# Optimization experiments

Hardware: AMD Instinct MI355X
Metric: run time of the kernel (lower is better)

Reference implementation:

```python
import jax, jax.numpy as jnp
import numpy as np

N, E, H, L = 50000, 800000, 64, 4
IN_NODE, IN_EDGE = 16, 8


def _lin(x, W, b=None):
    y = x @ W
    return y if b is None else y + b


def setup_inputs() -> dict:
    key = jax.random.key(0)
    ks = jax.random.split(key, 32)
    r = lambda i, shp, s=0.1: jax.random.normal(ks[i], shp, dtype=jnp.float32) * s
    inp = {
        "h": r(0, (N, IN_NODE), 1.0),
        "x": r(1, (N, 3), 1.0),
        "edge_attr": r(2, (E, IN_EDGE), 1.0),
        "node_mask": jnp.ones((N, 1), jnp.float32),
        "edge_mask": jnp.ones((E, 1), jnp.float32),
        # embedding linears
        "Wn_in": r(3, (IN_NODE, H)), "bn_in": r(4, (H,)),
        "Wn_out": r(5, (H, IN_NODE)), "bn_out": r(6, (IN_NODE,)),
        "We_in": r(7, (IN_EDGE, H)), "be_in": r(8, (H,)),
        "We_out": r(9, (H, IN_EDGE)), "be_out": r(10, (IN_EDGE,)),
        # per-layer E_GCL params (stacked over L layers)
        "eW1": r(11, (L, 2 * H + 1 + H, H)), "eb1": r(12, (L, H)),
        "eW2": r(13, (L, H, H)), "eb2": r(14, (L, H)),
        "nW1": r(15, (L, 2 * H, H)), "nb1": r(16, (L, H)),
        "nW2": r(17, (L, H, H)), "nb2": r(18, (L, H)),
        "cW1": r(19, (L, H, H)), "cb1": r(20, (L, H)),
        "cW2": r(21, (L, H, 1)),
        "edge_index": jax.random.randint(ks[22], (2, E), 0, N, dtype=jnp.int32),
    }
    return inp


def reference(h, x, edge_attr, node_mask, edge_mask,
              Wn_in, bn_in, Wn_out, bn_out, We_in, be_in, We_out, be_out,
              eW1, eb1, eW2, eb2, nW1, nb1, nW2, nb2, cW1, cb1, cW2,
              edge_index):
    silu = jax.nn.silu
    n = h.shape[0]
    row, col = edge_index[0], edge_index[1]
    h = _lin(h, Wn_in, bn_in)            # node embedding [N,H]
    e = _lin(edge_attr, We_in, be_in)    # edge embedding [E,H]
    for i in range(eW1.shape[0]):        # n_layers (structural loop)
        coord_diff = x[row] - x[col]                          # [E,3]
        radial = jnp.sum(coord_diff * coord_diff, -1, keepdims=True)  # [E,1]
        coord_diff = coord_diff / (jnp.sqrt(radial) + 1.0)    # norm_diff
        # edge model: gather -> MLP
        m = jnp.concatenate([h[row], h[col], radial, e], axis=-1)
        m = silu(_lin(m, eW1[i], eb1[i]))
        m = silu(_lin(m, eW2[i], eb2[i]))
        m = m * edge_mask
        # coord model (tanh=False, agg='sum'): scatter-add translations
        trans = coord_diff * _lin(silu(_lin(m, cW1[i], cb1[i])), cW2[i])
        x = x + jax.ops.segment_sum(trans, row, num_segments=n)
        # node model: scatter-add messages, MLP, residual (recurrent)
        agg = jax.ops.segment_sum(m, row, num_segments=n)
        out = _lin(silu(_lin(jnp.concatenate([h, agg], -1), nW1[i], nb1[i])), nW2[i], nb2[i])
        h = (h + out) * node_mask
        x = x * node_mask
        e = m  # edge_update: carry message as updated edge feature
    e = _lin(e, We_out, be_out) * edge_mask
    h = _lin(h, Wn_out, bn_out) * node_mask
    return h, x, e
```

## Files before the change

### kernel.cpp

```cpp
#include <hip/hip_runtime.h>

#define N_NODES 50000
#define N_EDGES 800000
#define NLAYERS 4
#define NTILES (N_EDGES / 64)
#define NTILES2 (N_EDGES / 128)

#define K1PAD 224
#define TPITCH 72
#define SCHUNK 49

typedef short bf16x8 __attribute__((ext_vector_type(8)));
typedef float f32x4 __attribute__((ext_vector_type(4)));

__device__ __forceinline__ unsigned short f2b(float f) {
  union { float f; unsigned int u; } v; v.f = f;
  unsigned int u = v.u;
  return (unsigned short)((u + 0x7fffu + ((u >> 16) & 1u)) >> 16);
}
__device__ __forceinline__ float b2f(unsigned short s) {
  union { unsigned int u; float f; } v; v.u = ((unsigned int)s) << 16;
  return v.f;
}
__device__ __forceinline__ float silu_f(float x) {
  return x / (1.0f + __expf(-x));
}

__global__ void k_hist(const int* __restrict__ eidx, int* __restrict__ cnt) {
  int e = blockIdx.x * 256 + threadIdx.x;
  if (e >= N_EDGES) return;
  atomicAdd(&cnt[eidx[e]], 1);
}
__global__ __launch_bounds__(1024) void k_scan(const int* __restrict__ cnt,
                                               int* __restrict__ rowptr,
                                               int* __restrict__ cur) {
  __shared__ int part[1024];
  const int t = threadIdx.x;
  const int base = t * SCHUNK;
  int s = 0;
  for (int i = 0; i < SCHUNK; i++) {
    int idx = base + i;
    s += (idx < N_NODES) ? cnt[idx] : 0;
  }
  part[t] = s;
  __syncthreads();
  for (int off = 1; off < 1024; off <<= 1) {
    int v = (t >= off) ? part[t - off] : 0;
    __syncthreads();
    part[t] += v;
    __syncthreads();
  }
  int run = (t == 0) ? 0 : part[t - 1];
  for (int i = 0; i < SCHUNK; i++) {
    int idx = base + i;
    if (idx < N_NODES) {
      rowptr[idx] = run;
      cur[idx] = run;
      run += cnt[idx];
    }
  }
  if (t == 1023) rowptr[N_NODES] = part[1023];
}
__global__ void k_scatter(const int* __restrict__ eidx, const float* __restrict__ emask,
                          int* __restrict__ cur, int* __restrict__ elist,
                          int* __restrict__ rs, int* __restrict__ cs,
                          float* __restrict__ msrt) {
  int e = blockIdx.x * 256 + threadIdx.x;
  if (e >= N_EDGES) return;
  int r = eidx[e], c = eidx[N_EDGES + e];
  int slot = atomicAdd(&cur[r], 1);
  elist[slot] = e;
  rs[slot] = r;
  cs[slot] = c;
  msrt[slot] = emask[e];
}

__global__ void k_convW1(const float* __restrict__ eW1, unsigned short* __restrict__ Wt1) {
  int id = blockIdx.x * 256 + threadIdx.x;
  if (id >= NLAYERS * 64 * K1PAD) return;
  int k = id % K1PAD; int rem = id / K1PAD; int o = rem % 64; int l = rem / 64;
  int src = (k < 128) ? k : (k < 192 ? k + 1 : (k == 192 ? 128 : -1));
  float v = (src >= 0) ? eW1[((size_t)l * 193 + src) * 64 + o] : 0.0f;
  Wt1[id] = f2b(v);
}
__global__ void k_convT(const float* __restrict__ W, unsigned short* __restrict__ Wt, int K) {
  int id = blockIdx.x * 256 + threadIdx.x;
  if (id >= NLAYERS * 64 * K) return;
  int k = id % K; int rem = id / K; int o = rem % 64; int l = rem / 64;
  Wt[id] = f2b(W[((size_t)l * K + k) * 64 + o]);
}
__global__ void k_convHead(const float* __restrict__ W, unsigned short* __restrict__ Wt, int O) {
  int id = blockIdx.x * 256 + threadIdx.x;
  if (id >= 16 * 64) return;
  int k = id & 63, o = id >> 6;
  Wt[id] = (o < O) ? f2b(W[(size_t)k * O + o]) : (unsigned short)0;
}

__global__ void k_h0(const float* __restrict__ hin, const float* __restrict__ W,
                     const float* __restrict__ b, float* __restrict__ h,
                     unsigned short* __restrict__ hbf) {
  int id = blockIdx.x * 256 + threadIdx.x;
  if (id >= N_NODES * 64) return;
  int n = id >> 6, j = id & 63;
  float s = b[j];
#pragma unroll
  for (int k = 0; k < 16; k++) s += hin[n * 16 + k] * W[k * 64 + j];
  h[id] = s;
  hbf[id] = f2b(s);
}
__global__ void k_e0(const float* __restrict__ ea, const float* __restrict__ W,
                     const float* __restrict__ b, const int* __restrict__ elist,
                     unsigned short* __restrict__ ebuf) {
  int id = blockIdx.x * 256 + threadIdx.x;
  if (id >= N_EDGES * 64) return;
  int pos = id >> 6, j = id & 63;
  int e = elist[pos];
  float s = b[j];
#pragma unroll
  for (int k = 0; k < 8; k++) s += ea[e * 8 + k] * W[k * 64 + j];
  ebuf[id] = f2b(s);
}

__global__ __launch_bounds__(256) void edge_kernel(
    const unsigned short* __restrict__ hbf, unsigned short* __restrict__ ebuf,
    const float* __restrict__ xin, float* __restrict__ xout,
    float* __restrict__ agg,
    const int* __restrict__ rs, const int* __restrict__ cs,
    const float* __restrict__ msrt,
    const unsigned short* __restrict__ Wt1,
    const unsigned short* __restrict__ Wt2,
    const unsigned short* __restrict__ Wtc,
    const float* __restrict__ eb1, const float* __restrict__ eb2,
    const float* __restrict__ cb1, const float* __restrict__ cw2) {
  __shared__ __attribute__((aligned(16))) unsigned short sT[128 * TPITCH];
  __shared__ __attribute__((aligned(16))) unsigned short sM[128 * TPITCH];
  __shared__ float sNdx[128 * 3];
  __shared__ float sMaskS[128];
  __shared__ int sRow[128];

  const int t = threadIdx.x;
  const int lane = t & 63, w = t >> 6;
  const int q = lane >> 4, li = lane & 15;
  const int rowA = w * 32 + li;
  const int rowB = rowA + 16;
  const int e0 = blockIdx.x * 128 + rowA;
  const int e1 = e0 + 16;

  const int rA = rs[e0], cA = cs[e0];
  const int rB = rs[e1], cB = cs[e1];

  float radA = 0.f, radB = 0.f;
  if (q == 0) {
    {
      float dx0 = xin[rA * 3 + 0] - xin[cA * 3 + 0];
      float dx1 = xin[rA * 3 + 1] - xin[cA * 3 + 1];
      float dx2 = xin[rA * 3 + 2] - xin[cA * 3 + 2];
      radA = dx0 * dx0 + dx1 * dx1 + dx2 * dx2;
      float inv = 1.0f / (sqrtf(radA) + 1.0f);
      sRow[rowA] = rA;
      sMaskS[rowA] = msrt[e0];
      sNdx[rowA * 3 + 0] = dx0 * inv;
      sNdx[rowA * 3 + 1] = dx1 * inv;
      sNdx[rowA * 3 + 2] = dx2 * inv;
    }
    {
      float dx0 = xin[rB * 3 + 0] - xin[cB * 3 + 0];
      float dx1 = xin[rB * 3 + 1] - xin[cB * 3 + 1];
      float dx2 = xin[rB * 3 + 2] - xin[cB * 3 + 2];
      radB = dx0 * dx0 + dx1 * dx1 + dx2 * dx2;
      float inv = 1.0f / (sqrtf(radB) + 1.0f);
      sRow[rowB] = rB;
      sMaskS[rowB] = msrt[e1];
      sNdx[rowB * 3 + 0] = dx0 * inv;
      sNdx[rowB * 3 + 1] = dx1 * inv;
      sNdx[rowB * 3 + 2] = dx2 * inv;
    }
  }

  const unsigned short* hrA = hbf + (size_t)rA * 64;
  const unsigned short* hcA = hbf + (size_t)cA * 64;
  const unsigned short* epA = ebuf + (size_t)e0 * 64;
  const unsigned short* hrB = hbf + (size_t)rB * 64;
  const unsigned short* hcB = hbf + (size_t)cB * 64;
  const unsigned short* epB = ebuf + (size_t)e1 * 64;

  f32x4 accA[4], accB[4];
  const f32x4 zero4 = {0.f, 0.f, 0.f, 0.f};
#pragma unroll
  for (int ct = 0; ct < 4; ct++) { accA[ct] = zero4; accB[ct] = zero4; }

  {
    bf16x8 afA[7], afB[7];
    afA[0] = *(const bf16x8*)(hrA + q * 8);
    afA[1] = *(const bf16x8*)(hrA + 32 + q * 8);
    afA[2] = *(const bf16x8*)(hcA + q * 8);
    afA[3] = *(const bf16x8*)(hcA + 32 + q * 8);
    afA[4] = *(const bf16x8*)(epA + q * 8);
    afA[5] = *(const bf16x8*)(epA + 32 + q * 8);
    afB[0] = *(const bf16x8*)(hrB + q * 8);
    afB[1] = *(const bf16x8*)(hrB + 32 + q * 8);
    afB[2] = *(const bf16x8*)(hcB + q * 8);
    afB[3] = *(const bf16x8*)(hcB + 32 + q * 8);
    afB[4] = *(const bf16x8*)(epB + q * 8);
    afB[5] = *(const bf16x8*)(epB + 32 + q * 8);
    bf16x8 a6A = {0, 0, 0, 0, 0, 0, 0, 0};
    bf16x8 a6B = {0, 0, 0, 0, 0, 0, 0, 0};
    if (q == 0) { a6A[0] = (short)f2b(radA); a6B[0] = (short)f2b(radB); }
    afA[6] = a6A; afB[6] = a6B;
#pragma unroll
    for (int ks = 0; ks < 7; ks++) {
      int kb = ks * 32 + q * 8;
#pragma unroll
      for (int ct = 0; ct < 4; ct++) {
        bf16x8 bfr = *(const bf16x8*)(Wt1 + (size_t)(ct * 16 + li) * K1PAD + kb);
        accA[ct] = __builtin_amdgcn_mfma_f32_16x16x32_bf16(afA[ks], bfr, accA[ct], 0, 0, 0);
        accB[ct] = __builtin_amdgcn_mfma_f32_16x16x32_bf16(afB[ks], bfr, accB[ct], 0, 0, 0);
      }
    }
  }
#pragma unroll
  for (int ct = 0; ct < 4; ct++) {
    float bias = eb1[ct * 16 + li];
#pragma unroll
    for (int r2 = 0; r2 < 4; r2++) {
      int elA = w * 32 + q * 4 + r2;
      sT[elA * TPITCH + ct * 16 + li] = f2b(silu_f(accA[ct][r2] + bias));
      sT[(elA + 16) * TPITCH + ct * 16 + li] = f2b(silu_f(accB[ct][r2] + bias));
    }
  }

#pragma unroll
  for (int ct = 0; ct < 4; ct++) { accA[ct] = zero4; accB[ct] = zero4; }
#pragma unroll
  for (int ks = 0; ks < 2; ks++) {
    int kb = ks * 32 + q * 8;
    bf16x8 afA = *(const bf16x8*)(sT + rowA * TPITCH + kb);
    bf16x8 afB = *(const bf16x8*)(sT + rowB * TPITCH + kb);
#pragma unroll
    for (int ct = 0; ct < 4; ct++) {
      bf16x8 bfr = *(const bf16x8*)(Wt2 + (size_t)(ct * 16 + li) * 64 + kb);
      accA[ct] = __builtin_amdgcn_mfma_f32_16x16x32_bf16(afA, bfr, accA[ct], 0, 0, 0);
      accB[ct] = __builtin_amdgcn_mfma_f32_16x16x32_bf16(afB, bfr, accB[ct], 0, 0, 0);
    }
  }
#pragma unroll
  for (int ct = 0; ct < 4; ct++) {
    float bias = eb2[ct * 16 + li];
#pragma unroll
    for (int r2 = 0; r2 < 4; r2++) {
      int elA = w * 32 + q * 4 + r2;
      int elB = elA + 16;
      float vA = silu_f(accA[ct][r2] + bias) * sMaskS[elA];
      float vB = silu_f(accB[ct][r2] + bias) * sMaskS[elB];
      sM[elA * TPITCH + ct * 16 + li] = f2b(vA);
      sM[elB * TPITCH + ct * 16 + li] = f2b(vB);
    }
  }

  {
    int el2 = t >> 1, part = t & 1;
    const uint4* src = (const uint4*)(sM + el2 * TPITCH + part * 32);
    uint4* dst = (uint4*)(ebuf + (size_t)(blockIdx.x * 128 + el2) * 64 + part * 32);
    dst[0] = src[0]; dst[1] = src[1]; dst[2] = src[2]; dst[3] = src[3];
  }

  {
    float accv = 0.f;
    int curRow = sRow[w * 32];
#pragma unroll
    for (int i = 0; i < 32; i++) {
      int rr = sRow[w * 32 + i];
      float v = b2f(sM[(w * 32 + i) * TPITCH + lane]);
      if (rr != curRow) {
        atomicAdd(&agg[(size_t)curRow * 64 + lane], accv);
        accv = 0.f;
        curRow = rr;
      }
      accv += v;
    }
    atomicAdd(&agg[(size_t)curRow * 64 + lane], accv);
  }

#pragma unroll
  for (int ct = 0; ct < 4; ct++) { accA[ct] = zero4; accB[ct] = zero4; }
#pragma unroll
  for (int ks = 0; ks < 2; ks++) {
    int kb = ks * 32 + q * 8;
    bf16x8 afA = *(const bf16x8*)(sM + rowA * TPITCH + kb);
    bf16x8 afB = *(const bf16x8*)(sM + rowB * TPITCH + kb);
#pragma unroll
    for (int ct = 0; ct < 4; ct++) {
      bf16x8 bfr = *(const bf16x8*)(Wtc + (size_t)(ct * 16 + li) * 64 + kb);
      accA[ct] = __builtin_amdgcn_mfma_f32_16x16x32_bf16(afA, bfr, accA[ct], 0, 0, 0);
      accB[ct] = __builtin_amdgcn_mfma_f32_16x16x32_bf16(afB, bfr, accB[ct], 0, 0, 0);
    }
  }
  float pA[4] = {0.f, 0.f, 0.f, 0.f};
  float pB[4] = {0.f, 0.f, 0.f, 0.f};
#pragma unroll
  for (int ct = 0; ct < 4; ct++) {
    float bias = cb1[ct * 16 + li];
    float wv = cw2[ct * 16 + li];
#pragma unroll
    for (int r2 = 0; r2 < 4; r2++) {
      pA[r2] += silu_f(accA[ct][r2] + bias) * wv;
      pB[r2] += silu_f(accB[ct][r2] + bias) * wv;
    }
  }
#pragma unroll
  for (int m = 1; m < 16; m <<= 1) {
#pragma unroll
    for (int r2 = 0; r2 < 4; r2++) {
      pA[r2] += __shfl_xor(pA[r2], m, 64);
      pB[r2] += __shfl_xor(pB[r2], m, 64);
    }
  }
  if (li < 3) {
    {
      int el0 = w * 32 + q * 4;
      float accx = sNdx[el0 * 3 + li] * pA[0];
      int cr = sRow[el0];
#pragma unroll
      for (int r2 = 1; r2 < 4; r2++) {
        int el = el0 + r2;
        int rr = sRow[el];
        float tv = sNdx[el * 3 + li] * pA[r2];
        if (rr != cr) {
          atomicAdd(&xout[(size_t)cr * 3 + li], accx);
          accx = 0.f;
          cr = rr;
        }
        accx += tv;
      }
      atomicAdd(&xout[(size_t)cr * 3 + li], accx);
    }
    {
      int el0 = w * 32 + 16 + q * 4;
      float accx = sNdx[el0 * 3 + li] * pB[0];
      int cr = sRow[el0];
#pragma unroll
      for (int r2 = 1; r2 < 4; r2++) {
        int el = el0 + r2;
        int rr = sRow[el];
        float tv = sNdx[el * 3 + li] * pB[r2];
        if (rr != cr) {
          atomicAdd(&xout[(size_t)cr * 3 + li], accx);
          accx = 0.f;
          cr = rr;
        }
        accx += tv;
      }
      atomicAdd(&xout[(size_t)cr * 3 + li], accx);
    }
  }
}

__global__ __launch_bounds__(256) void node_kernel(
    float* __restrict__ h, unsigned short* __restrict__ hbf,
    const float* __restrict__ agg,
    float* __restrict__ xout, const float* __restrict__ nmask,
    const unsigned short* __restrict__ Wtn1,
    const unsigned short* __restrict__ Wtn2,
    const float* __restrict__ nb1, const float* __restrict__ nb2) {
  __shared__ __attribute__((aligned(16))) unsigned short sT[64 * TPITCH];
  const int t = threadIdx.x;
  const int nb = blockIdx.x * 64;

  if (t < 192) {
    int n2 = nb + t / 3, c2 = t % 3;
    if (n2 < N_NODES) xout[(size_t)n2 * 3 + c2] *= nmask[n2];
  }

  const int lane = t & 63, w = t >> 6;
  const int q = lane >> 4, li = lane & 15;
  const int nrow = w * 16 + li;
  const int n = nb + nrow;
  const bool valid = (n < N_NODES);
  const f32x4 zero4 = {0.f, 0.f, 0.f, 0.f};

  f32x4 acc[4];
#pragma unroll
  for (int ct = 0; ct < 4; ct++) acc[ct] = zero4;

  {
    bf16x8 afs[4];
    const bf16x8 az = {0, 0, 0, 0, 0, 0, 0, 0};
    if (valid) {
      afs[0] = *(const bf16x8*)(hbf + (size_t)n * 64 + q * 8);
      afs[1] = *(const bf16x8*)(hbf + (size_t)n * 64 + 32 + q * 8);
      const float* ap = agg + (size_t)n * 64;
      bf16x8 a2, a3;
#pragma unroll
      for (int j = 0; j < 8; j++) {
        a2[j] = (short)f2b(ap[q * 8 + j]);
        a3[j] = (short)f2b(ap[32 + q * 8 + j]);
      }
      afs[2] = a2; afs[3] = a3;
    } else {
      afs[0] = az; afs[1] = az; afs[2] = az; afs[3] = az;
    }
#pragma unroll
    for (int ks = 0; ks < 4; ks++) {
      int kb = ks * 32 + q * 8;
#pragma unroll
      for (int ct = 0; ct < 4; ct++) {
        bf16x8 bfr = *(const bf16x8*)(Wtn1 + (size_t)(ct * 16 + li) * 128 + kb);
        acc[ct] = __builtin_amdgcn_mfma_f32_16x16x32_bf16(afs[ks], bfr, acc[ct], 0, 0, 0);
      }
    }
  }
#pragma unroll
  for (int ct = 0; ct < 4; ct++) {
    float bias = nb1[ct * 16 + li];
#pragma unroll
    for (int r2 = 0; r2 < 4; r2++) {
      int nl = w * 16 + q * 4 + r2;
      sT[nl * TPITCH + ct * 16 + li] = f2b(silu_f(acc[ct][r2] + bias));
    }
  }

#pragma unroll
  for (int ct = 0; ct < 4; ct++) acc[ct] = zero4;
#pragma unroll
  for (int ks = 0; ks < 2; ks++) {
    int kb = ks * 32 + q * 8;
    bf16x8 af = *(const bf16x8*)(sT + nrow * TPITCH + kb);
#pragma unroll
    for (int ct = 0; ct < 4; ct++) {
      bf16x8 bfr = *(const bf16x8*)(Wtn2 + (size_t)(ct * 16 + li) * 64 + kb);
      acc[ct] = __builtin_amdgcn_mfma_f32_16x16x32_bf16(af, bfr, acc[ct], 0, 0, 0);
    }
  }
#pragma unroll
  for (int ct = 0; ct < 4; ct++) {
    float bias = nb2[ct * 16 + li];
#pragma unroll
    for (int r2 = 0; r2 < 4; r2++) {
      int node = nb + w * 16 + q * 4 + r2;
      if (node < N_NODES) {
        float nm = nmask[node];
        size_t o = (size_t)node * 64 + ct * 16 + li;
        float hv = (h[o] + acc[ct][r2] + bias) * nm;
        h[o] = hv;
        hbf[o] = f2b(hv);
      }
    }
  }
}

__global__ __launch_bounds__(256) void k_hout(const unsigned short* __restrict__ hbf,
                                              const unsigned short* __restrict__ WoT,
                                              const float* __restrict__ b,
                                              const float* __restrict__ nmask,
                                              float* __restrict__ out) {
  const int t = threadIdx.x, lane = t & 63, w = t >> 6;
  const int q = lane >> 4, li = lane & 15;
  const int nb = blockIdx.x * 64;
  const int n = nb + w * 16 + li;
  const bf16x8 az = {0, 0, 0, 0, 0, 0, 0, 0};
  bf16x8 a0 = az, a1 = az;
  if (n < N_NODES) {
    a0 = *(const bf16x8*)(hbf + (size_t)n * 64 + q * 8);
    a1 = *(const bf16x8*)(hbf + (size_t)n * 64 + 32 + q * 8);
  }
  bf16x8 b0 = *(const bf16x8*)(WoT + li * 64 + q * 8);
  bf16x8 b1 = *(const bf16x8*)(WoT + li * 64 + 32 + q * 8);
  f32x4 acc = {0.f, 0.f, 0.f, 0.f};
  acc = __builtin_amdgcn_mfma_f32_16x16x32_bf16(a0, b0, acc, 0, 0, 0);
  acc = __builtin_amdgcn_mfma_f32_16x16x32_bf16(a1, b1, acc, 0, 0, 0);
  float bias = b[li];
#pragma unroll
  for (int r2 = 0; r2 < 4; r2++) {
    int node = nb + w * 16 + q * 4 + r2;
    if (node < N_NODES) out[(size_t)node * 16 + li] = (acc[r2] + bias) * nmask[node];
  }
}
__global__ __launch_bounds__(256) void k_eout(const unsigned short* __restrict__ ebuf,
                                              const unsigned short* __restrict__ WoT,
                                              const float* __restrict__ b,
                                              const float* __restrict__ emask,
                                              const int* __restrict__ elist,
                                              float* __restrict__ out) {
  const int t = threadIdx.x, lane = t & 63, w = t >> 6;
  const int q = lane >> 4, li = lane & 15;
  const int eb0 = blockIdx.x * 64;
  const int e = eb0 + w * 16 + li;
  bf16x8 a0 = *(const bf16x8*)(ebuf + (size_t)e * 64 + q * 8);
  bf16x8 a1 = *(const bf16x8*)(ebuf + (size_t)e * 64 + 32 + q * 8);
  bf16x8 b0 = *(const bf16x8*)(WoT + li * 64 + q * 8);
  bf16x8 b1 = *(const bf16x8*)(WoT + li * 64 + 32 + q * 8);
  f32x4 acc = {0.f, 0.f, 0.f, 0.f};
  acc = __builtin_amdgcn_mfma_f32_16x16x32_bf16(a0, b0, acc, 0, 0, 0);
  acc = __builtin_amdgcn_mfma_f32_16x16x32_bf16(a1, b1, acc, 0, 0, 0);
  if (li < 8) {
    float bias = b[li];
#pragma unroll
    for (int r2 = 0; r2 < 4; r2++) {
      int ee = eb0 + w * 16 + q * 4 + r2;
      int orig = elist[ee];
      out[(size_t)orig * 8 + li] = (acc[r2] + bias) * emask[orig];
    }
  }
}

extern "C" void kernel_launch(void* const* d_in, const int* in_sizes, int n_in,
                              void* d_out, int out_size, void* d_ws, size_t ws_size,
                              hipStream_t stream) {
  (void)in_sizes; (void)n_in; (void)out_size; (void)ws_size;
  const float* in_h   = (const float*)d_in[0];
  const float* in_x   = (const float*)d_in[1];
  const float* in_ea  = (const float*)d_in[2];
  const float* nmask  = (const float*)d_in[3];
  const float* emask  = (const float*)d_in[4];
  const float* Wn_in  = (const float*)d_in[5];
  const float* bn_in  = (const float*)d_in[6];
  const float* Wn_out = (const float*)d_in[7];
  const float* bn_out = (const float*)d_in[8];
  const float* We_in  = (const float*)d_in[9];
  const float* be_in  = (const float*)d_in[10];
  const float* We_out = (const float*)d_in[11];
  const float* be_out = (const float*)d_in[12];
  const float* eW1    = (const float*)d_in[13];
  const float* eb1    = (const float*)d_in[14];
  const float* eW2    = (const float*)d_in[15];
  const float* eb2    = (const float*)d_in[16];
  const float* nW1    = (const float*)d_in[17];
  const float* nb1    = (const float*)d_in[18];
  const float* nW2    = (const float*)d_in[19];
  const float* nb2    = (const float*)d_in[20];
  const float* cW1    = (const float*)d_in[21];
  const float* cb1    = (const float*)d_in[22];
  const float* cW2    = (const float*)d_in[23];
  const int*   eidx   = (const int*)d_in[24];

  char* ws = (char*)d_ws;
  size_t off = 0;
  auto alloc = [&](size_t bytes) {
    size_t o = off; off = (off + bytes + 255) & ~(size_t)255; return (void*)(ws + o);
  };
  float* h             = (float*)alloc((size_t)N_NODES * 64 * 4);
  unsigned short* hbf  = (unsigned short*)alloc((size_t)N_NODES * 64 * 2);
  unsigned short* ebuf = (unsigned short*)alloc((size_t)N_EDGES * 64 * 2);
  float* agg           = (float*)alloc((size_t)N_NODES * 64 * 4);
  float* xb0           = (float*)alloc((size_t)N_NODES * 3 * 4);
  float* xb1           = (float*)alloc((size_t)N_NODES * 3 * 4);
  int* cnt             = (int*)alloc((size_t)N_NODES * 4);
  int* rowptr          = (int*)alloc((size_t)(N_NODES + 1) * 4);
  int* cur             = (int*)alloc((size_t)N_NODES * 4);
  int* elist           = (int*)alloc((size_t)N_EDGES * 4);
  int* rsorted         = (int*)alloc((size_t)N_EDGES * 4);
  int* csorted         = (int*)alloc((size_t)N_EDGES * 4);
  float* msorted       = (float*)alloc((size_t)N_EDGES * 4);
  unsigned short* Wt1  = (unsigned short*)alloc((size_t)NLAYERS * 64 * K1PAD * 2);
  unsigned short* Wt2  = (unsigned short*)alloc((size_t)NLAYERS * 64 * 64 * 2);
  unsigned short* Wtc  = (unsigned short*)alloc((size_t)NLAYERS * 64 * 64 * 2);
  unsigned short* Wtn1 = (unsigned short*)alloc((size_t)NLAYERS * 64 * 128 * 2);
  unsigned short* Wtn2 = (unsigned short*)alloc((size_t)NLAYERS * 64 * 64 * 2);
  unsigned short* WoN  = (unsigned short*)alloc((size_t)16 * 64 * 2);
  unsigned short* WoE  = (unsigned short*)alloc((size_t)16 * 64 * 2);

  hipMemsetAsync(cnt, 0, (size_t)N_NODES * 4, stream);
  k_hist<<<(N_EDGES + 255) / 256, 256, 0, stream>>>(eidx, cnt);
  k_scan<<<1, 1024, 0, stream>>>(cnt, rowptr, cur);
  k_scatter<<<(N_EDGES + 255) / 256, 256, 0, stream>>>(eidx, emask, cur, elist,
                                                       rsorted, csorted, msorted);

  k_convW1<<<(NLAYERS * 64 * K1PAD + 255) / 256, 256, 0, stream>>>(eW1, Wt1);
  k_convT<<<(NLAYERS * 64 * 64 + 255) / 256, 256, 0, stream>>>(eW2, Wt2, 64);
  k_convT<<<(NLAYERS * 64 * 64 + 255) / 256, 256, 0, stream>>>(cW1, Wtc, 64);
  k_convT<<<(NLAYERS * 64 * 128 + 255) / 256, 256, 0, stream>>>(nW1, Wtn1, 128);
  k_convT<<<(NLAYERS * 64 * 64 + 255) / 256, 256, 0, stream>>>(nW2, Wtn2, 64);
  k_convHead<<<4, 256, 0, stream>>>(Wn_out, WoN, 16);
  k_convHead<<<4, 256, 0, stream>>>(We_out, WoE, 8);

  k_h0<<<(N_NODES * 64 + 255) / 256, 256, 0, stream>>>(in_h, Wn_in, bn_in, h, hbf);
  k_e0<<<(N_EDGES * 64 + 255) / 256, 256, 0, stream>>>(in_ea, We_in, be_in, elist, ebuf);
  hipMemcpyAsync(xb0, in_x, (size_t)N_NODES * 3 * 4, hipMemcpyDeviceToDevice, stream);

  for (int l = 0; l < NLAYERS; l++) {
    float* xi = (l & 1) ? xb1 : xb0;
    float* xo = (l & 1) ? xb0 : xb1;
    hipMemsetAsync(agg, 0, (size_t)N_NODES * 64 * 4, stream);
    hipMemcpyAsync(xo, xi, (size_t)N_NODES * 3 * 4, hipMemcpyDeviceToDevice, stream);
    edge_kernel<<<NTILES2, 256, 0, stream>>>(
        hbf, ebuf, xi, xo, agg, rsorted, csorted, msorted,
        Wt1 + (size_t)l * 64 * K1PAD, Wt2 + (size_t)l * 64 * 64, Wtc + (size_t)l * 64 * 64,
        eb1 + l * 64, eb2 + l * 64, cb1 + l * 64, cW2 + l * 64);
    node_kernel<<<(N_NODES + 63) / 64, 256, 0, stream>>>(
        h, hbf, agg, xo, nmask,
        Wtn1 + (size_t)l * 64 * 128, Wtn2 + (size_t)l * 64 * 64, nb1 + l * 64, nb2 + l * 64);
  }

  float* out = (float*)d_out;
  k_hout<<<(N_NODES + 63) / 64, 256, 0, stream>>>(hbf, WoN, bn_out, nmask, out);
  k_eout<<<NTILES, 256, 0, stream>>>(ebuf, WoE, be_out, emask, elist, out + 950000);
  hipMemcpyAsync(out + 800000, xb0, (size_t)N_NODES * 3 * 4, hipMemcpyDeviceToDevice, stream);
}
```

Measured before the change: 1.325 ms.

## Give each wave 64 edges, double node tile, zero agg in node kernel

The edge kernel now runs 128 threads per block, so each wave handles four 16-edge tiles instead of two. Each weight fragment loaded feeds four MFMAs, and the segmented scatter runs over longer runs of sorted edges. The node kernel processes 128 nodes per block with two tiles per wave and zeroes the agg rows after reading them, which replaces the per-layer memset with a single initial one. The cost is much higher register pressure (16 accumulators and 28 A fragments per lane) and fewer waves per block, which may lower occupancy or cause spills.

New measurement: 1.572 ms. +18.7%, slower.

```diff
diff --git a/kernel.cpp b/kernel.cpp
--- a/kernel.cpp
+++ b/kernel.cpp
@@ -4,7 +4,9 @@
 #define N_EDGES 800000
 #define NLAYERS 4
 #define NTILES (N_EDGES / 64)
-#define NTILES2 (N_EDGES / 128)
+
+#define EB 128
+#define EDGE_GRID (N_EDGES / EB)
 
 #define K1PAD 224
 #define TPITCH 72
@@ -121,7 +123,7 @@
   ebuf[id] = f2b(s);
 }
 
-__global__ __launch_bounds__(256) void edge_kernel(
+__global__ __launch_bounds__(128) void edge_kernel(
     const unsigned short* __restrict__ hbf, unsigned short* __restrict__ ebuf,
     const float* __restrict__ xin, float* __restrict__ xout,
     float* __restrict__ agg,
@@ -132,89 +134,78 @@
     const unsigned short* __restrict__ Wtc,
     const float* __restrict__ eb1, const float* __restrict__ eb2,
     const float* __restrict__ cb1, const float* __restrict__ cw2) {
-  __shared__ __attribute__((aligned(16))) unsigned short sT[128 * TPITCH];
-  __shared__ __attribute__((aligned(16))) unsigned short sM[128 * TPITCH];
-  __shared__ float sNdx[128 * 3];
-  __shared__ float sMaskS[128];
-  __shared__ int sRow[128];
+  __shared__ __attribute__((aligned(16))) unsigned short sT[EB * TPITCH];
+  __shared__ __attribute__((aligned(16))) unsigned short sM[EB * TPITCH];
+  __shared__ float sNdx[EB * 3];
+  __shared__ float sMaskS[EB];
+  __shared__ int sRow[EB];
 
   const int t = threadIdx.x;
   const int lane = t & 63, w = t >> 6;
   const int q = lane >> 4, li = lane & 15;
-  const int rowA = w * 32 + li;
-  const int rowB = rowA + 16;
-  const int e0 = blockIdx.x * 128 + rowA;
-  const int e1 = e0 + 16;
-
-  const int rA = rs[e0], cA = cs[e0];
-  const int rB = rs[e1], cB = cs[e1];
-
-  float radA = 0.f, radB = 0.f;
+  const int base = w * 64;
+  const int eglob = blockIdx.x * EB;
+
+  int rr[4], cc[4];
+#pragma unroll
+  for (int tt = 0; tt < 4; tt++) {
+    int el = base + tt * 16 + li;
+    rr[tt] = rs[eglob + el];
+    cc[tt] = cs[eglob + el];
+  }
+
+  float rad[4] = {0.f, 0.f, 0.f, 0.f};
   if (q == 0) {
-    {
-      float dx0 = xin[rA * 3 + 0] - xin[cA * 3 + 0];
-      float dx1 = xin[rA * 3 + 1] - xin[cA * 3 + 1];
-      float dx2 = xin[rA * 3 + 2] - xin[cA * 3 + 2];
-      radA = dx0 * dx0 + dx1 * dx1 + dx2 * dx2;
-      float inv = 1.0f / (sqrtf(radA) + 1.0f);
-      sRow[rowA] = rA;
-      sMaskS[rowA] = msrt[e0];
-      sNdx[rowA * 3 + 0] = dx0 * inv;
-      sNdx[rowA * 3 + 1] = dx1 * inv;
-      sNdx[rowA * 3 + 2] = dx2 * inv;
-    }
-    {
-      float dx0 = xin[rB * 3 + 0] - xin[cB * 3 + 0];
-      float dx1 = xin[rB * 3 + 1] - xin[cB * 3 + 1];
-      float dx2 = xin[rB * 3 + 2] - xin[cB * 3 + 2];
-      radB = dx0 * dx0 + dx1 * dx1 + dx2 * dx2;
-      float inv = 1.0f / (sqrtf(radB) + 1.0f);
-      sRow[rowB] = rB;
-      sMaskS[rowB] = msrt[e1];
-      sNdx[rowB * 3 + 0] = dx0 * inv;
-      sNdx[rowB * 3 + 1] = dx1 * inv;
-      sNdx[rowB * 3 + 2] = dx2 * inv;
-    }
-  }
-
-  const unsigned short* hrA = hbf + (size_t)rA * 64;
-  const unsigned short* hcA = hbf + (size_t)cA * 64;
-  const unsigned short* epA = ebuf + (size_t)e0 * 64;
-  const unsigned short* hrB = hbf + (size_t)rB * 64;
-  const unsigned short* hcB = hbf + (size_t)cB * 64;
-  const unsigned short* epB = ebuf + (size_t)e1 * 64;
-
-  f32x4 accA[4], accB[4];
+#pragma unroll
+    for (int tt = 0; tt < 4; tt++) {
+      int el = base + tt * 16 + li;
+      float dx0 = xin[rr[tt] * 3 + 0] - xin[cc[tt] * 3 + 0];
+      float dx1 = xin[rr[tt] * 3 + 1] - xin[cc[tt] * 3 + 1];
+      float dx2 = xin[rr[tt] * 3 + 2] - xin[cc[tt] * 3 + 2];
+      float rv = dx0 * dx0 + dx1 * dx1 + dx2 * dx2;
+      rad[tt] = rv;
+      float inv = 1.0f / (sqrtf(rv) + 1.0f);
+      sRow[el] = rr[tt];
+      sMaskS[el] = msrt[eglob + el];
+      sNdx[el * 3 + 0] = dx0 * inv;
+      sNdx[el * 3 + 1] = dx1 * inv;
+      sNdx[el * 3 + 2] = dx2 * inv;
+    }
+  }
+
+  f32x4 acc[4][4];
   const f32x4 zero4 = {0.f, 0.f, 0.f, 0.f};
 #pragma unroll
-  for (int ct = 0; ct < 4; ct++) { accA[ct] = zero4; accB[ct] = zero4; }
+  for (int tt = 0; tt < 4; tt++)
+#pragma unroll
+    for (int ct = 0; ct < 4; ct++) acc[tt][ct] = zero4;
 
   {
-    bf16x8 afA[7], afB[7];
-    afA[0] = *(const bf16x8*)(hrA + q * 8);
-    afA[1] = *(const bf16x8*)(hrA + 32 + q * 8);
-    afA[2] = *(const bf16x8*)(hcA + q * 8);
-    afA[3] = *(const bf16x8*)(hcA + 32 + q * 8);
-    afA[4] = *(const bf16x8*)(epA + q * 8);
-    afA[5] = *(const bf16x8*)(epA + 32 + q * 8);
-    afB[0] = *(const bf16x8*)(hrB + q * 8);
-    afB[1] = *(const bf16x8*)(hrB + 32 + q * 8);
-    afB[2] = *(const bf16x8*)(hcB + q * 8);
-    afB[3] = *(const bf16x8*)(hcB + 32 + q * 8);
-    afB[4] = *(const bf16x8*)(epB + q * 8);
-    afB[5] = *(const bf16x8*)(epB + 32 + q * 8);
-    bf16x8 a6A = {0, 0, 0, 0, 0, 0, 0, 0};
-    bf16x8 a6B = {0, 0, 0, 0, 0, 0, 0, 0};
-    if (q == 0) { a6A[0] = (short)f2b(radA); a6B[0] = (short)f2b(radB); }
-    afA[6] = a6A; afB[6] = a6B;
+    bf16x8 af[4][7];
+#pragma unroll
+    for (int tt = 0; tt < 4; tt++) {
+      const unsigned short* hr = hbf + (size_t)rr[tt] * 64;
+      const unsigned short* hc = hbf + (size_t)cc[tt] * 64;
+      const unsigned short* ep = ebuf + (size_t)(eglob + base + tt * 16 + li) * 64;
+      af[tt][0] = *(const bf16x8*)(hr + q * 8);
+      af[tt][1] = *(const bf16x8*)(hr + 32 + q * 8);
+      af[tt][2] = *(const bf16x8*)(hc + q * 8);
+      af[tt][3] = *(const bf16x8*)(hc + 32 + q * 8);
+      af[tt][4] = *(const bf16x8*)(ep + q * 8);
+      af[tt][5] = *(const bf16x8*)(ep + 32 + q * 8);
+      bf16x8 a6 = {0, 0, 0, 0, 0, 0, 0, 0};
+      if (q == 0) a6[0] = (short)f2b(rad[tt]);
+      af[tt][6] = a6;
+    }
 #pragma unroll
     for (int ks = 0; ks < 7; ks++) {
       int kb = ks * 32 + q * 8;
 #pragma unroll
       for (int ct = 0; ct < 4; ct++) {
         bf16x8 bfr = *(const bf16x8*)(Wt1 + (size_t)(ct * 16 + li) * K1PAD + kb);
-        accA[ct] = __builtin_amdgcn_mfma_f32_16x16x32_bf16(afA[ks], bfr, accA[ct], 0, 0, 0);
-        accB[ct] = __builtin_amdgcn_mfma_f32_16x16x32_bf16(afB[ks], bfr, accB[ct], 0, 0, 0);
+#pragma unroll
+        for (int tt = 0; tt < 4; tt++)
+          acc[tt][ct] = __builtin_amdgcn_mfma_f32_16x16x32_bf16(af[tt][ks], bfr, acc[tt][ct], 0, 0, 0);
       }
     }
   }
@@ -223,24 +214,31 @@
     float bias = eb1[ct * 16 + li];
 #pragma unroll
     for (int r2 = 0; r2 < 4; r2++) {
-      int elA = w * 32 + q * 4 + r2;
-      sT[elA * TPITCH + ct * 16 + li] = f2b(silu_f(accA[ct][r2] + bias));
-      sT[(elA + 16) * TPITCH + ct * 16 + li] = f2b(silu_f(accB[ct][r2] + bias));
-    }
-  }
-
-#pragma unroll
-  for (int ct = 0; ct < 4; ct++) { accA[ct] = zero4; accB[ct] = zero4; }
+#pragma unroll
+      for (int tt = 0; tt < 4; tt++) {
+        int el = base + tt * 16 + q * 4 + r2;
+        sT[el * TPITCH + ct * 16 + li] = f2b(silu_f(acc[tt][ct][r2] + bias));
+      }
+    }
+  }
+
+#pragma unroll
+  for (int tt = 0; tt < 4; tt++)
+#pragma unroll
+    for (int ct = 0; ct < 4; ct++) acc[tt][ct] = zero4;
 #pragma unroll
   for (int ks = 0; ks < 2; ks++) {
     int kb = ks * 32 + q * 8;
-    bf16x8 afA = *(const bf16x8*)(sT + rowA * TPITCH + kb);
-    bf16x8 afB = *(const bf16x8*)(sT + rowB * TPITCH + kb);
+    bf16x8 af[4];
+#pragma unroll
+    for (int tt = 0; tt < 4; tt++)
+      af[tt] = *(const bf16x8*)(sT + (base + tt * 16 + li) * TPITCH + kb);
 #pragma unroll
     for (int ct = 0; ct < 4; ct++) {
       bf16x8 bfr = *(const bf16x8*)(Wt2 + (size_t)(ct * 16 + li) * 64 + kb);
-      accA[ct] = __builtin_amdgcn_mfma_f32_16x16x32_bf16(afA, bfr, accA[ct], 0, 0, 0);
-      accB[ct] = __builtin_amdgcn_mfma_f32_16x16x32_bf16(afB, bfr, accB[ct], 0, 0, 0);
+#pragma unroll
+      for (int tt = 0; tt < 4; tt++)
+        acc[tt][ct] = __builtin_amdgcn_mfma_f32_16x16x32_bf16(af[tt], bfr, acc[tt][ct], 0, 0, 0);
     }
   }
 #pragma unroll
@@ -248,33 +246,35 @@
     float bias = eb2[ct * 16 + li];
 #pragma unroll
     for (int r2 = 0; r2 < 4; r2++) {
-      int elA = w * 32 + q * 4 + r2;
-      int elB = elA + 16;
-      float vA = silu_f(accA[ct][r2] + bias) * sMaskS[elA];
-      float vB = silu_f(accB[ct][r2] + bias) * sMaskS[elB];
-      sM[elA * TPITCH + ct * 16 + li] = f2b(vA);
-      sM[elB * TPITCH + ct * 16 + li] = f2b(vB);
-    }
-  }
-
-  {
-    int el2 = t >> 1, part = t & 1;
+#pragma unroll
+      for (int tt = 0; tt < 4; tt++) {
+        int el = base + tt * 16 + q * 4 + r2;
+        float v = silu_f(acc[tt][ct][r2] + bias) * sMaskS[el];
+        sM[el * TPITCH + ct * 16 + li] = f2b(v);
+      }
+    }
+  }
+
+#pragma unroll
+  for (int pass = 0; pass < 2; pass++) {
+    int el2 = base + pass * 32 + (lane >> 1);
+    int part = lane & 1;
     const uint4* src = (const uint4*)(sM + el2 * TPITCH + part * 32);
-    uint4* dst = (uint4*)(ebuf + (size_t)(blockIdx.x * 128 + el2) * 64 + part * 32);
+    uint4* dst = (uint4*)(ebuf + (size_t)(eglob + el2) * 64 + part * 32);
     dst[0] = src[0]; dst[1] = src[1]; dst[2] = src[2]; dst[3] = src[3];
   }
 
   {
     float accv = 0.f;
-    int curRow = sRow[w * 32];
-#pragma unroll
-    for (int i = 0; i < 32; i++) {
-      int rr = sRow[w * 32 + i];
-      float v = b2f(sM[(w * 32 + i) * TPITCH + lane]);
-      if (rr != curRow) {
+    int curRow = sRow[base];
+#pragma unroll
+    for (int i = 0; i < 64; i++) {
+      int rrow = sRow[base + i];
+      float v = b2f(sM[(base + i) * TPITCH + lane]);
+      if (rrow != curRow) {
         atomicAdd(&agg[(size_t)curRow * 64 + lane], accv);
         accv = 0.f;
-        curRow = rr;
+        curRow = rrow;
       }
       accv += v;
     }
@@ -282,131 +282,129 @@
   }
 
 #pragma unroll
-  for (int ct = 0; ct < 4; ct++) { accA[ct] = zero4; accB[ct] = zero4; }
+  for (int tt = 0; tt < 4; tt++)
+#pragma unroll
+    for (int ct = 0; ct < 4; ct++) acc[tt][ct] = zero4;
 #pragma unroll
   for (int ks = 0; ks < 2; ks++) {
     int kb = ks * 32 + q * 8;
-    bf16x8 afA = *(const bf16x8*)(sM + rowA * TPITCH + kb);
-    bf16x8 afB = *(const bf16x8*)(sM + rowB * TPITCH + kb);
+    bf16x8 af[4];
+#pragma unroll
+    for (int tt = 0; tt < 4; tt++)
+      af[tt] = *(const bf16x8*)(sM + (base + tt * 16 + li) * TPITCH + kb);
 #pragma unroll
     for (int ct = 0; ct < 4; ct++) {
       bf16x8 bfr = *(const bf16x8*)(Wtc + (size_t)(ct * 16 + li) * 64 + kb);
-      accA[ct] = __builtin_amdgcn_mfma_f32_16x16x32_bf16(afA, bfr, accA[ct], 0, 0, 0);
-      accB[ct] = __builtin_amdgcn_mfma_f32_16x16x32_bf16(afB, bfr, accB[ct], 0, 0, 0);
-    }
-  }
-  float pA[4] = {0.f, 0.f, 0.f, 0.f};
-  float pB[4] = {0.f, 0.f, 0.f, 0.f};
+#pragma unroll
+      for (int tt = 0; tt < 4; tt++)
+        acc[tt][ct] = __builtin_amdgcn_mfma_f32_16x16x32_bf16(af[tt], bfr, acc[tt][ct], 0, 0, 0);
+    }
+  }
+  float p[4][4];
+#pragma unroll
+  for (int tt = 0; tt < 4; tt++)
+#pragma unroll
+    for (int r2 = 0; r2 < 4; r2++) p[tt][r2] = 0.f;
 #pragma unroll
   for (int ct = 0; ct < 4; ct++) {
     float bias = cb1[ct * 16 + li];
     float wv = cw2[ct * 16 + li];
 #pragma unroll
-    for (int r2 = 0; r2 < 4; r2++) {
-      pA[r2] += silu_f(accA[ct][r2] + bias) * wv;
-      pB[r2] += silu_f(accB[ct][r2] + bias) * wv;
-    }
+    for (int tt = 0; tt < 4; tt++)
+#pragma unroll
+      for (int r2 = 0; r2 < 4; r2++)
+        p[tt][r2] += silu_f(acc[tt][ct][r2] + bias) * wv;
   }
 #pragma unroll
   for (int m = 1; m < 16; m <<= 1) {
 #pragma unroll
-    for (int r2 = 0; r2 < 4; r2++) {
-      pA[r2] += __shfl_xor(pA[r2], m, 64);
-      pB[r2] += __shfl_xor(pB[r2], m, 64);
-    }
+    for (int tt = 0; tt < 4; tt++)
+#pragma unroll
+      for (int r2 = 0; r2 < 4; r2++) p[tt][r2] += __shfl_xor(p[tt][r2], m, 64);
   }
   if (li < 3) {
-    {
-      int el0 = w * 32 + q * 4;
-      float accx = sNdx[el0 * 3 + li] * pA[0];
+#pragma unroll
+    for (int tt = 0; tt < 4; tt++) {
+      int el0 = base + tt * 16 + q * 4;
+      float accx = sNdx[el0 * 3 + li] * p[tt][0];
       int cr = sRow[el0];
 #pragma unroll
       for (int r2 = 1; r2 < 4; r2++) {
         int el = el0 + r2;
-        int rr = sRow[el];
-        float tv = sNdx[el * 3 + li] * pA[r2];
-        if (rr != cr) {
+        int rrow = sRow[el];
+        float tv = sNdx[el * 3 + li] * p[tt][r2];
+        if (rrow != cr) {
           atomicAdd(&xout[(size_t)cr * 3 + li], accx);
           accx = 0.f;
-          cr = rr;
+          cr = rrow;
         }
         accx += tv;
       }
       atomicAdd(&xout[(size_t)cr * 3 + li], accx);
     }
-    {
-      int el0 = w * 32 + 16 + q * 4;
-      float accx = sNdx[el0 * 3 + li] * pB[0];
-      int cr = sRow[el0];
-#pragma unroll
-      for (int r2 = 1; r2 < 4; r2++) {
-        int el = el0 + r2;
-        int rr = sRow[el];
-        float tv = sNdx[el * 3 + li] * pB[r2];
-        if (rr != cr) {
-          atomicAdd(&xout[(size_t)cr * 3 + li], accx);
-          accx = 0.f;
-          cr = rr;
-        }
-        accx += tv;
-      }
-      atomicAdd(&xout[(size_t)cr * 3 + li], accx);
-    }
   }
 }
 
 __global__ __launch_bounds__(256) void node_kernel(
     float* __restrict__ h, unsigned short* __restrict__ hbf,
-    const float* __restrict__ agg,
+    float* __restrict__ agg,
     float* __restrict__ xout, const float* __restrict__ nmask,
     const unsigned short* __restrict__ Wtn1,
     const unsigned short* __restrict__ Wtn2,
     const float* __restrict__ nb1, const float* __restrict__ nb2) {
-  __shared__ __attribute__((aligned(16))) unsigned short sT[64 * TPITCH];
+  __shared__ __attribute__((aligned(16))) unsigned short sT[128 * TPITCH];
   const int t = threadIdx.x;
-  const int nb = blockIdx.x * 64;
-
-  if (t < 192) {
-    int n2 = nb + t / 3, c2 = t % 3;
+  const int nb = blockIdx.x * 128;
+
+  for (int i = t; i < 128 * 3; i += 256) {
+    int n2 = nb + i / 3, c2 = i % 3;
     if (n2 < N_NODES) xout[(size_t)n2 * 3 + c2] *= nmask[n2];
   }
 
   const int lane = t & 63, w = t >> 6;
   const int q = lane >> 4, li = lane & 15;
-  const int nrow = w * 16 + li;
-  const int n = nb + nrow;
-  const bool valid = (n < N_NODES);
   const f32x4 zero4 = {0.f, 0.f, 0.f, 0.f};
-
-  f32x4 acc[4];
-#pragma unroll
-  for (int ct = 0; ct < 4; ct++) acc[ct] = zero4;
-
-  {
-    bf16x8 afs[4];
-    const bf16x8 az = {0, 0, 0, 0, 0, 0, 0, 0};
-    if (valid) {
-      afs[0] = *(const bf16x8*)(hbf + (size_t)n * 64 + q * 8);
-      afs[1] = *(const bf16x8*)(hbf + (size_t)n * 64 + 32 + q * 8);
-      const float* ap = agg + (size_t)n * 64;
+  const float4 f4z = make_float4(0.f, 0.f, 0.f, 0.f);
+
+  f32x4 acc[2][4];
+#pragma unroll
+  for (int tt = 0; tt < 2; tt++)
+#pragma unroll
+    for (int ct = 0; ct < 4; ct++) acc[tt][ct] = zero4;
+
+  bf16x8 af[2][4];
+  const bf16x8 az = {0, 0, 0, 0, 0, 0, 0, 0};
+#pragma unroll
+  for (int tt = 0; tt < 2; tt++) {
+    int n = nb + w * 32 + tt * 16 + li;
+    if (n < N_NODES) {
+      af[tt][0] = *(const bf16x8*)(hbf + (size_t)n * 64 + q * 8);
+      af[tt][1] = *(const bf16x8*)(hbf + (size_t)n * 64 + 32 + q * 8);
+      float* ap = agg + (size_t)n * 64;
       bf16x8 a2, a3;
 #pragma unroll
       for (int j = 0; j < 8; j++) {
         a2[j] = (short)f2b(ap[q * 8 + j]);
         a3[j] = (short)f2b(ap[32 + q * 8 + j]);
       }
-      afs[2] = a2; afs[3] = a3;
+      af[tt][2] = a2; af[tt][3] = a3;
+      *(float4*)(ap + q * 8) = f4z;
+      *(float4*)(ap + q * 8 + 4) = f4z;
+      *(float4*)(ap + 32 + q * 8) = f4z;
+      *(float4*)(ap + 32 + q * 8 + 4) = f4z;
     } else {
-      afs[0] = az; afs[1] = az; afs[2] = az; afs[3] = az;
-    }
-#pragma unroll
-    for (int ks = 0; ks < 4; ks++) {
-      int kb = ks * 32 + q * 8;
-#pragma unroll
-      for (int ct = 0; ct < 4; ct++) {
-        bf16x8 bfr = *(const bf16x8*)(Wtn1 + (size_t)(ct * 16 + li) * 128 + kb);
-        acc[ct] = __builtin_amdgcn_mfma_f32_16x16x32_bf16(afs[ks], bfr, acc[ct], 0, 0, 0);
-      }
+      af[tt][0] = az; af[tt][1] = az; af[tt][2] = az; af[tt][3] = az;
+    }
+  }
+#pragma unroll
+  for (int ks = 0; ks < 4; ks++) {
+    int kb = ks * 32 + q * 8;
+#pragma unroll
+    for (int ct = 0; ct < 4; ct++) {
+      bf16x8 bfr = *(const bf16x8*)(Wtn1 + (size_t)(ct * 16 + li) * 128 + kb);
+#pragma unroll
+      for (int tt = 0; tt < 2; tt++)
+        acc[tt][ct] = __builtin_amdgcn_mfma_f32_16x16x32_bf16(af[tt][ks], bfr, acc[tt][ct], 0, 0, 0);
     }
   }
 #pragma unroll
@@ -414,21 +412,31 @@
     float bias = nb1[ct * 16 + li];
 #pragma unroll
     for (int r2 = 0; r2 < 4; r2++) {
-      int nl = w * 16 + q * 4 + r2;
-      sT[nl * TPITCH + ct * 16 + li] = f2b(silu_f(acc[ct][r2] + bias));
-    }
-  }
-
-#pragma unroll
-  for (int ct = 0; ct < 4; ct++) acc[ct] = zero4;
+#pragma unroll
+      for (int tt = 0; tt < 2; tt++) {
+        int nl = w * 32 + tt * 16 + q * 4 + r2;
+        sT[nl * TPITCH + ct * 16 + li] = f2b(silu_f(acc[tt][ct][r2] + bias));
+      }
+    }
+  }
+
+#pragma unroll
+  for (int tt = 0; tt < 2; tt++)
+#pragma unroll
+    for (int ct = 0; ct < 4; ct++) acc[tt][ct] = zero4;
 #pragma unroll
   for (int ks = 0; ks < 2; ks++) {
     int kb = ks * 32 + q * 8;
-    bf16x8 af = *(const bf16x8*)(sT + nrow * TPITCH + kb);
+    bf16x8 afr[2];
+#pragma unroll
+    for (int tt = 0; tt < 2; tt++)
+      afr[tt] = *(const bf16x8*)(sT + (w * 32 + tt * 16 + li) * TPITCH + kb);
 #pragma unroll
     for (int ct = 0; ct < 4; ct++) {
       bf16x8 bfr = *(const bf16x8*)(Wtn2 + (size_t)(ct * 16 + li) * 64 + kb);
-      acc[ct] = __builtin_amdgcn_mfma_f32_16x16x32_bf16(af, bfr, acc[ct], 0, 0, 0);
+#pragma unroll
+      for (int tt = 0; tt < 2; tt++)
+        acc[tt][ct] = __builtin_amdgcn_mfma_f32_16x16x32_bf16(afr[tt], bfr, acc[tt][ct], 0, 0, 0);
     }
   }
 #pragma unroll
@@ -436,13 +444,16 @@
     float bias = nb2[ct * 16 + li];
 #pragma unroll
     for (int r2 = 0; r2 < 4; r2++) {
-      int node = nb + w * 16 + q * 4 + r2;
-      if (node < N_NODES) {
-        float nm = nmask[node];
-        size_t o = (size_t)node * 64 + ct * 16 + li;
-        float hv = (h[o] + acc[ct][r2] + bias) * nm;
-        h[o] = hv;
-        hbf[o] = f2b(hv);
+#pragma unroll
+      for (int tt = 0; tt < 2; tt++) {
+        int node = nb + w * 32 + tt * 16 + q * 4 + r2;
+        if (node < N_NODES) {
+          float nm = nmask[node];
+          size_t o = (size_t)node * 64 + ct * 16 + li;
+          float hv = (h[o] + acc[tt][ct][r2] + bias) * nm;
+          h[o] = hv;
+          hbf[o] = f2b(hv);
+        }
       }
     }
   }
@@ -576,17 +587,17 @@
   k_h0<<<(N_NODES * 64 + 255) / 256, 256, 0, stream>>>(in_h, Wn_in, bn_in, h, hbf);
   k_e0<<<(N_EDGES * 64 + 255) / 256, 256, 0, stream>>>(in_ea, We_in, be_in, elist, ebuf);
   hipMemcpyAsync(xb0, in_x, (size_t)N_NODES * 3 * 4, hipMemcpyDeviceToDevice, stream);
+  hipMemsetAsync(agg, 0, (size_t)N_NODES * 64 * 4, stream);
 
   for (int l = 0; l < NLAYERS; l++) {
     float* xi = (l & 1) ? xb1 : xb0;
     float* xo = (l & 1) ? xb0 : xb1;
-    hipMemsetAsync(agg, 0, (size_t)N_NODES * 64 * 4, stream);
     hipMemcpyAsync(xo, xi, (size_t)N_NODES * 3 * 4, hipMemcpyDeviceToDevice, stream);
-    edge_kernel<<<NTILES2, 256, 0, stream>>>(
+    edge_kernel<<<EDGE_GRID, 128, 0, stream>>>(
         hbf, ebuf, xi, xo, agg, rsorted, csorted, msorted,
         Wt1 + (size_t)l * 64 * K1PAD, Wt2 + (size_t)l * 64 * 64, Wtc + (size_t)l * 64 * 64,
         eb1 + l * 64, eb2 + l * 64, cb1 + l * 64, cW2 + l * 64);
-    node_kernel<<<(N_NODES + 63) / 64, 256, 0, stream>>>(
+    node_kernel<<<(N_NODES + 127) / 128, 256, 0, stream>>>(
         h, hbf, agg, xo, nmask,
         Wtn1 + (size_t)l * 64 * 128, Wtn2 + (size_t)l * 64 * 64, nb1 + l * 64, nb2 + l * 64);
   }
```
